# Optimization experiments

Hardware: AMD Instinct MI355X
Metric: run time of the kernel (lower is better)

The kernel has to match this reference:

```python
import jax, jax.numpy as jnp
import numpy as np

NEG_SLOPE = 0.01  # torch.nn.LeakyReLU default


def setup_inputs() -> dict:
    key = jax.random.key(0)
    ks = jax.random.split(key, 9)
    B, S, F1, F2, N, M, E, L = 2, 256, 512, 512, 20000, 2, 320000, 3
    x = jax.random.normal(ks[0], (B, S, F1), dtype=jnp.float32)
    nodes = jax.random.normal(ks[1], (N, M, F2), dtype=jnp.float32)
    edge_index = jax.random.randint(ks[2], (2, E), 0, N, dtype=jnp.int32)
    Wp = jax.random.normal(ks[3], (F1, F2), dtype=jnp.float32) * 0.02  # torch Linear weight [out,in]
    bp = jax.random.normal(ks[4], (F1,), dtype=jnp.float32) * 0.02
    gcn_W = jax.random.normal(ks[5], (L, S, S), dtype=jnp.float32) * 0.05  # stored as [in,out]
    gcn_b = jax.random.normal(ks[6], (L, S), dtype=jnp.float32) * 0.02
    w_bp = jax.random.normal(ks[7], (S,), dtype=jnp.float32) * 0.05
    b_bp = jax.random.normal(ks[8], (1,), dtype=jnp.float32) * 0.02
    return {"x": x, "nodes": nodes, "edge_index": edge_index, "Wp": Wp, "bp": bp,
            "gcn_W": gcn_W, "gcn_b": gcn_b, "w_bp": w_bp, "b_bp": b_bp}


def reference(x, nodes, edge_index, Wp, bp, gcn_W, gcn_b, w_bp, b_bp):
    # Eval mode: dropout layers are identity.
    N = nodes.shape[0]
    L = gcn_W.shape[0]
    proj = nodes @ Wp.T + bp                         # [N, M, F1]
    score = jnp.einsum('bsk,nmk->bsn', x, proj)      # sum over M and F1 -> [B, S, N]
    h = score.transpose(0, 2, 1)                     # beliefs [B, N, S]

    # GCN normalization with self-loops: D^{-1/2} (A + I) D^{-1/2}
    src, dst = edge_index[0], edge_index[1]
    loop = jnp.arange(N, dtype=edge_index.dtype)
    row = jnp.concatenate([src, loop])               # message sources
    col = jnp.concatenate([dst, loop])               # message targets
    deg = jnp.zeros((N,), dtype=h.dtype).at[col].add(1.0)
    dinv = deg ** -0.5                               # deg >= 1 due to self-loops
    norm = dinv[row] * dinv[col]                     # [E+N]

    for l in range(L):
        hw = h @ gcn_W[l]                            # [B, N, S]
        msg = hw[:, row, :] * norm[None, :, None]    # gather + scale
        agg = jnp.zeros_like(hw).at[:, col, :].add(msg) + gcn_b[l]
        h = jax.nn.leaky_relu(agg, NEG_SLOPE)

    # belief_projection: Linear(S, 1) then squeeze -> [B, N]
    return h @ w_bp + b_bp[0]
```

## Files before the change

### kernel.cpp

```cpp
#include <hip/hip_runtime.h>
#include <cstddef>
#include <cstdint>

#define NN 20000
#define SDIM 256

typedef short frag16 __attribute__((ext_vector_type(8)));
typedef float f32x4 __attribute__((ext_vector_type(4)));

__device__ inline unsigned short f32_to_bf16(float f) {
    uint32_t u = __float_as_uint(f);
    u += 0x7FFFu + ((u >> 16) & 1u);
    return (unsigned short)(u >> 16);
}

__device__ inline float4 dec4(uint2 v) {
    float4 r;
    r.x = __uint_as_float(v.x << 16);
    r.y = __uint_as_float(v.x & 0xffff0000u);
    r.z = __uint_as_float(v.y << 16);
    r.w = __uint_as_float(v.y & 0xffff0000u);
    return r;
}

__global__ __launch_bounds__(256) void prep(
    const float* __restrict__ nodes, const float* __restrict__ x,
    const float* __restrict__ Wp, const float* __restrict__ gcn_W,
    const int* __restrict__ src, const int* __restrict__ dst,
    unsigned short* __restrict__ nsum16, unsigned short* __restrict__ Wpb,
    unsigned short* __restrict__ WT, unsigned short* __restrict__ Tb,
    int* __restrict__ cnt, int* __restrict__ csr, int E)
{
    __shared__ __align__(16) char shmem[8704];
    const int blk = blockIdx.x, tid = threadIdx.x;

    if (blk < 64) {
        float* As = (float*)shmem;
        float* Bs = As + 1024;
        int b = blk >> 5, rem = blk & 31;
        int s0 = (rem >> 3) * 64, f0 = (rem & 7) * 64;
        const float* W1 = gcn_W;
        const float* xb = x + (size_t)b * 256 * 512;
        int kk = tid >> 4, c4 = (tid & 15) << 2;
        int tm = tid >> 4, tn = tid & 15;
        float acc[4][4] = {};
        for (int k0 = 0; k0 < 256; k0 += 16) {
            float4 av = *(const float4*)(W1 + (size_t)(k0 + kk) * 256 + s0 + c4);
            float4 bv = *(const float4*)(xb + (size_t)(k0 + kk) * 512 + f0 + c4);
            __syncthreads();
            *(float4*)&As[kk * 64 + c4] = av;
            *(float4*)&Bs[kk * 64 + c4] = bv;
            __syncthreads();
            #pragma unroll
            for (int k = 0; k < 16; ++k) {
                float a[4], bb[4];
                *(float4*)a  = *(const float4*)&As[k * 64 + (tm << 2)];
                *(float4*)bb = *(const float4*)&Bs[k * 64 + (tn << 2)];
                #pragma unroll
                for (int i = 0; i < 4; ++i)
                    #pragma unroll
                    for (int j = 0; j < 4; ++j) acc[i][j] += a[i] * bb[j];
            }
        }
        #pragma unroll
        for (int i = 0; i < 4; ++i) {
            int row = b * 256 + s0 + (tm << 2) + i;
            ushort4 o;
            o.x = f32_to_bf16(acc[i][0]); o.y = f32_to_bf16(acc[i][1]);
            o.z = f32_to_bf16(acc[i][2]); o.w = f32_to_bf16(acc[i][3]);
            *(ushort4*)(Tb + (size_t)row * 512 + f0 + (tn << 2)) = o;
        }
    } else if (blk < 10112) {
        int idx = (blk - 64) * 256 + tid;
        int n = idx >> 7, k4 = (idx & 127) << 2;
        uint2 o;
        if (n < NN) {
            float4 a = *(const float4*)(nodes + (size_t)n * 1024 + k4);
            float4 b = *(const float4*)(nodes + (size_t)n * 1024 + 512 + k4);
            o.x = ((uint32_t)f32_to_bf16(a.y + b.y) << 16) | f32_to_bf16(a.x + b.x);
            o.y = ((uint32_t)f32_to_bf16(a.w + b.w) << 16) | f32_to_bf16(a.z + b.z);
        } else { o.x = 0; o.y = 0; }
        *(uint2*)(nsum16 + (size_t)idx * 4) = o;
    } else if (blk < 10240) {
        size_t off = ((size_t)(blk - 10112) * 256 + tid) * 8;
        float4 a = *(const float4*)(Wp + off);
        float4 b = *(const float4*)(Wp + off + 4);
        uint4 o;
        o.x = ((uint32_t)f32_to_bf16(a.y) << 16) | f32_to_bf16(a.x);
        o.y = ((uint32_t)f32_to_bf16(a.w) << 16) | f32_to_bf16(a.z);
        o.z = ((uint32_t)f32_to_bf16(b.y) << 16) | f32_to_bf16(b.x);
        o.w = ((uint32_t)f32_to_bf16(b.w) << 16) | f32_to_bf16(b.z);
        *(uint4*)(Wpb + off) = o;
    } else if (blk < 10272) {
        unsigned short (*tsh)[68] = (unsigned short(*)[68])shmem;
        int t = blk - 10240;
        int l = t >> 4, rem = t & 15;
        int c0 = (rem & 3) * 64, r0 = (rem >> 2) * 64;
        const float* inp = gcn_W + (size_t)(l + 1) * 65536;
        unsigned short* outp = WT + (size_t)l * 65536;
        int tx = tid & 15, ty = tid >> 4;
        #pragma unroll
        for (int rr = 0; rr < 4; ++rr) {
            int r = ty * 4 + rr;
            float4 v = *(const float4*)(inp + (size_t)(r0 + r) * 256 + c0 + tx * 4);
            tsh[tx * 4 + 0][r] = f32_to_bf16(v.x);
            tsh[tx * 4 + 1][r] = f32_to_bf16(v.y);
            tsh[tx * 4 + 2][r] = f32_to_bf16(v.z);
            tsh[tx * 4 + 3][r] = f32_to_bf16(v.w);
        }
        __syncthreads();
        #pragma unroll
        for (int cc = 0; cc < 4; ++cc) {
            int c = ty * 4 + cc;
            ushort4 o = *(ushort4*)&tsh[c][tx * 4];
            *(ushort4*)(outp + (size_t)(c0 + c) * 256 + r0 + tx * 4) = o;
        }
    } else {
        int e = (blk - 10272) * 256 + tid;
        if (e < E) {
            int d = dst[e];
            int pos = atomicAdd(&cnt[d], 1);
            if (pos < 64) csr[(d << 6) + pos] = src[e];
        }
    }
}

__global__ __launch_bounds__(256) void mgemm(
    const unsigned short* __restrict__ A, const unsigned short* __restrict__ BT,
    int K, int N, int mode,
    const float* __restrict__ cb2, const int* __restrict__ cnt,
    unsigned short* __restrict__ C,
    float* __restrict__ cb2out, const float* __restrict__ bp,
    const unsigned short* __restrict__ Tb)
{
    if (mode == 0 && (int)blockIdx.y == 157) {
        int idx = blockIdx.x * 256 + threadIdx.x;
        if (idx < 512) {
            const unsigned short* tr = Tb + (size_t)idx * 512;
            float s = 0.f;
            for (int k = 0; k < 512; k += 8) {
                uint4 u = *(const uint4*)(tr + k);
                float4 a = dec4(make_uint2(u.x, u.y)), b = dec4(make_uint2(u.z, u.w));
                float4 p0 = *(const float4*)(bp + k);
                float4 p1 = *(const float4*)(bp + k + 4);
                s += a.x * p0.x + a.y * p0.y + a.z * p0.z + a.w * p0.w
                   + b.x * p1.x + b.y * p1.y + b.z * p1.z + b.w * p1.w;
            }
            cb2out[idx] = 2.0f * s;
        }
        return;
    }

    __shared__ __align__(16) unsigned short As[128 * 32];
    __shared__ __align__(16) unsigned short Bs[128 * 32];
    const int bm = blockIdx.y * 128, bn = blockIdx.x * 128;
    const int tid = threadIdx.x;
    const int lane = tid & 63, w = tid >> 6;
    const int wm = (w >> 1) << 6, wn = (w & 1) << 6;
    const int r = lane & 15, q = lane >> 4;

    f32x4 acc[4][4] = {};

    for (int k0 = 0; k0 < K; k0 += 32) {
        __syncthreads();
        #pragma unroll
        for (int t = 0; t < 2; ++t) {
            int c = t * 256 + w * 64 + lane;
            int row = c >> 2, col = (c & 3) << 3;
            __builtin_amdgcn_global_load_lds(
                (const __attribute__((address_space(1))) void*)(A + (size_t)(bm + row) * K + k0 + col),
                (__attribute__((address_space(3))) void*)(As + (size_t)(t * 256 + w * 64) * 8),
                16, 0, 0);
            __builtin_amdgcn_global_load_lds(
                (const __attribute__((address_space(1))) void*)(BT + (size_t)(bn + row) * K + k0 + col),
                (__attribute__((address_space(3))) void*)(Bs + (size_t)(t * 256 + w * 64) * 8),
                16, 0, 0);
        }
        __syncthreads();
        frag16 af[4], bf[4];
        #pragma unroll
        for (int i = 0; i < 4; ++i)
            af[i] = *(const frag16*)(As + ((wm + i * 16 + r) << 5) + (q << 3));
        #pragma unroll
        for (int j = 0; j < 4; ++j)
            bf[j] = *(const frag16*)(Bs + ((wn + j * 16 + r) << 5) + (q << 3));
        #pragma unroll
        for (int i = 0; i < 4; ++i)
            #pragma unroll
            for (int j = 0; j < 4; ++j)
                acc[i][j] = __builtin_amdgcn_mfma_f32_16x16x32_bf16(af[i], bf[j], acc[i][j], 0, 0, 0);
    }

    #pragma unroll
    for (int i = 0; i < 4; ++i) {
        #pragma unroll
        for (int rg = 0; rg < 4; ++rg) {
            int m = bm + wm + i * 16 + (q << 2) + rg;
            float sc = 1.0f;
            int b2 = 0, node = m;
            if (mode == 1) {
                int nc = m > NN - 1 ? NN - 1 : m;
                sc = rsqrtf((float)cnt[nc] + 1.0f);
            } else if (mode == 2) {
                b2 = m >= NN;
                node = m - b2 * NN;
                int nc = node > NN - 1 ? NN - 1 : node;
                sc = rsqrtf((float)cnt[nc] + 1.0f);
            }
            #pragma unroll
            for (int j = 0; j < 4; ++j) {
                int n = bn + wn + j * 16 + r;
                if (mode == 1) {
                    float v = (acc[i][j][rg] + cb2[n]) * sc;
                    C[(size_t)m * 512 + n] = f32_to_bf16(v);
                } else if (mode == 2) {
                    float v = acc[i][j][rg] * sc;
                    C[(size_t)node * 512 + (b2 << 8) + n] = f32_to_bf16(v);
                } else {
                    C[(size_t)m * N + n] = f32_to_bf16(acc[i][j][rg]);
                }
            }
        }
    }
}

__global__ __launch_bounds__(256) void aggregate_i(
    const unsigned short* __restrict__ hw, const int* __restrict__ cnt,
    const int* __restrict__ csr, const float* __restrict__ bias,
    unsigned short* __restrict__ hout,
    const float* __restrict__ w_bp, const float* __restrict__ b_bp,
    float* __restrict__ out)
{
    int n = blockIdx.x * 4 + (threadIdx.x >> 6);
    int lane = threadIdx.x & 63;
    const unsigned short* rowp = hw + (lane << 3);

    float acc[8];
    {
        uint4 u = *(const uint4*)(rowp + (size_t)n * 512);
        float4 a = dec4(make_uint2(u.x, u.y)), b = dec4(make_uint2(u.z, u.w));
        acc[0] = a.x; acc[1] = a.y; acc[2] = a.z; acc[3] = a.w;
        acc[4] = b.x; acc[5] = b.y; acc[6] = b.z; acc[7] = b.w;
    }
    int deg = cnt[n]; if (deg > 64) deg = 64;
    const int* cp = csr + (n << 6);
    int e = 0;
    for (; e + 8 <= deg; e += 8) {
        uint4 u[8];
        #pragma unroll
        for (int t = 0; t < 8; ++t)
            u[t] = *(const uint4*)(rowp + (size_t)cp[e + t] * 512);
        #pragma unroll
        for (int t = 0; t < 8; ++t) {
            float4 a = dec4(make_uint2(u[t].x, u[t].y)), b = dec4(make_uint2(u[t].z, u[t].w));
            acc[0] += a.x; acc[1] += a.y; acc[2] += a.z; acc[3] += a.w;
            acc[4] += b.x; acc[5] += b.y; acc[6] += b.z; acc[7] += b.w;
        }
    }
    if (e + 4 <= deg) {
        uint4 u[4];
        #pragma unroll
        for (int t = 0; t < 4; ++t)
            u[t] = *(const uint4*)(rowp + (size_t)cp[e + t] * 512);
        #pragma unroll
        for (int t = 0; t < 4; ++t) {
            float4 a = dec4(make_uint2(u[t].x, u[t].y)), b = dec4(make_uint2(u[t].z, u[t].w));
            acc[0] += a.x; acc[1] += a.y; acc[2] += a.z; acc[3] += a.w;
            acc[4] += b.x; acc[5] += b.y; acc[6] += b.z; acc[7] += b.w;
        }
        e += 4;
    }
    for (; e < deg; ++e) {
        uint4 u = *(const uint4*)(rowp + (size_t)cp[e] * 512);
        float4 a = dec4(make_uint2(u.x, u.y)), b = dec4(make_uint2(u.z, u.w));
        acc[0] += a.x; acc[1] += a.y; acc[2] += a.z; acc[3] += a.w;
        acc[4] += b.x; acc[5] += b.y; acc[6] += b.z; acc[7] += b.w;
    }

    float dn = rsqrtf((float)deg + 1.0f);
    int s = (lane & 31) << 3;
    float4 bl0 = *(const float4*)(bias + s);
    float4 bl1 = *(const float4*)(bias + s + 4);
    float v[8];
    v[0] = fmaf(dn, acc[0], bl0.x); v[1] = fmaf(dn, acc[1], bl0.y);
    v[2] = fmaf(dn, acc[2], bl0.z); v[3] = fmaf(dn, acc[3], bl0.w);
    v[4] = fmaf(dn, acc[4], bl1.x); v[5] = fmaf(dn, acc[5], bl1.y);
    v[6] = fmaf(dn, acc[6], bl1.z); v[7] = fmaf(dn, acc[7], bl1.w);
    #pragma unroll
    for (int j = 0; j < 8; ++j) v[j] = v[j] > 0.f ? v[j] : 0.01f * v[j];

    int b = lane >> 5;
    if (out) {
        float4 w0 = *(const float4*)(w_bp + s);
        float4 w1 = *(const float4*)(w_bp + s + 4);
        float sum = v[0] * w0.x + v[1] * w0.y + v[2] * w0.z + v[3] * w0.w
                  + v[4] * w1.x + v[5] * w1.y + v[6] * w1.z + v[7] * w1.w;
        #pragma unroll
        for (int off = 16; off; off >>= 1) sum += __shfl_xor(sum, off);
        if ((lane & 31) == 0) out[b * NN + n] = sum + b_bp[0];
    } else {
        uint4 o;
        o.x = ((uint32_t)f32_to_bf16(v[1]) << 16) | f32_to_bf16(v[0]);
        o.y = ((uint32_t)f32_to_bf16(v[3]) << 16) | f32_to_bf16(v[2]);
        o.z = ((uint32_t)f32_to_bf16(v[5]) << 16) | f32_to_bf16(v[4]);
        o.w = ((uint32_t)f32_to_bf16(v[7]) << 16) | f32_to_bf16(v[6]);
        *(uint4*)(hout + ((size_t)(b * NN + n)) * 256 + s) = o;
    }
}

extern "C" void kernel_launch(void* const* d_in, const int* in_sizes, int n_in,
                              void* d_out, int out_size, void* d_ws, size_t ws_size,
                              hipStream_t stream) {
    const float* x     = (const float*)d_in[0];
    const float* nodes = (const float*)d_in[1];
    const int*   eidx  = (const int*)d_in[2];
    const float* Wp    = (const float*)d_in[3];
    const float* bp    = (const float*)d_in[4];
    const float* gcn_W = (const float*)d_in[5];
    const float* gcn_b = (const float*)d_in[6];
    const float* w_bp  = (const float*)d_in[7];
    const float* b_bp  = (const float*)d_in[8];
    const int E = in_sizes[2] / 2;

    char* w = (char*)d_ws;
    auto alloc = [&](size_t bytes) { char* p = w; w += (bytes + 255) & ~(size_t)255; return p; };
    unsigned short* nsum16 = (unsigned short*)alloc((size_t)20096 * 512 * 2);
    unsigned short* Z      = (unsigned short*)alloc((size_t)20096 * 512 * 2);
    unsigned short* hA     = (unsigned short*)alloc((size_t)40192 * 256 * 2);
    unsigned short* hB     = (unsigned short*)alloc((size_t)40192 * 256 * 2);
    unsigned short* Wpb = (unsigned short*)alloc((size_t)512 * 512 * 2);
    unsigned short* Tb  = (unsigned short*)alloc((size_t)512 * 512 * 2);
    unsigned short* WT  = (unsigned short*)alloc((size_t)2 * 256 * 256 * 2);
    float* cb2 = (float*)alloc(512 * 4);
    int*   cnt = (int*)alloc((size_t)NN * 4);
    int*   csr = (int*)alloc((size_t)NN * 64 * 4);
    unsigned short* hw16 = nsum16;

    hipMemsetAsync(cnt, 0, (size_t)NN * 4, stream);

    const int cntBlks = (E + 255) / 256;
    prep<<<10272 + cntBlks, 256, 0, stream>>>(nodes, x, Wp, gcn_W, eidx, eidx + E,
                                              nsum16, Wpb, WT, Tb, cnt, csr, E);

    mgemm<<<dim3(4, 158), 256, 0, stream>>>(nsum16, Wpb, 512, 512, 0,
                                            nullptr, cnt, Z, cb2, bp, Tb);
    mgemm<<<dim3(4, 157), 256, 0, stream>>>(Z, Tb, 512, 512, 1,
                                            cb2, cnt, hw16, nullptr, nullptr, nullptr);

    aggregate_i<<<5000, 256, 0, stream>>>(hw16, cnt, csr, gcn_b + 0, hA,
                                          w_bp, b_bp, nullptr);
    mgemm<<<dim3(2, 313), 256, 0, stream>>>(hA, WT, 256, 256, 2,
                                            nullptr, cnt, hw16, nullptr, nullptr, nullptr);
    aggregate_i<<<5000, 256, 0, stream>>>(hw16, cnt, csr, gcn_b + 256, hB,
                                          w_bp, b_bp, nullptr);
    mgemm<<<dim3(2, 313), 256, 0, stream>>>(hB, WT + 65536, 256, 256, 2,
                                            nullptr, cnt, hw16, nullptr, nullptr, nullptr);
    aggregate_i<<<5000, 256, 0, stream>>>(hw16, cnt, csr, gcn_b + 512, nullptr,
                                          w_bp, b_bp, (float*)d_out);
}
```

Measured before the change: 393.2 us.

## Reassociate projection chain to fold Wp into small matrix, drop big GEMM

```diff
diff --git a/kernel.cpp b/kernel.cpp
--- a/kernel.cpp
+++ b/kernel.cpp
@@ -3,7 +3,6 @@
 #include <cstdint>
 
 #define NN 20000
-#define SDIM 256
 
 typedef short frag16 __attribute__((ext_vector_type(8)));
 typedef float f32x4 __attribute__((ext_vector_type(4)));
@@ -25,10 +24,10 @@
 
 __global__ __launch_bounds__(256) void prep(
     const float* __restrict__ nodes, const float* __restrict__ x,
-    const float* __restrict__ Wp, const float* __restrict__ gcn_W,
+    const float* __restrict__ gcn_W, const float* __restrict__ bp,
     const int* __restrict__ src, const int* __restrict__ dst,
-    unsigned short* __restrict__ nsum16, unsigned short* __restrict__ Wpb,
-    unsigned short* __restrict__ WT, unsigned short* __restrict__ Tb,
+    unsigned short* __restrict__ nsum16, unsigned short* __restrict__ WT,
+    float* __restrict__ Tf, float* __restrict__ cvec,
     int* __restrict__ cnt, int* __restrict__ csr, int E)
 {
     __shared__ __align__(16) char shmem[8704];
@@ -65,35 +64,36 @@
         #pragma unroll
         for (int i = 0; i < 4; ++i) {
             int row = b * 256 + s0 + (tm << 2) + i;
-            ushort4 o;
-            o.x = f32_to_bf16(acc[i][0]); o.y = f32_to_bf16(acc[i][1]);
-            o.z = f32_to_bf16(acc[i][2]); o.w = f32_to_bf16(acc[i][3]);
-            *(ushort4*)(Tb + (size_t)row * 512 + f0 + (tn << 2)) = o;
-        }
-    } else if (blk < 10112) {
-        int idx = (blk - 64) * 256 + tid;
-        int n = idx >> 7, k4 = (idx & 127) << 2;
-        uint2 o;
+            *(float4*)(Tf + (size_t)row * 512 + f0 + (tn << 2)) =
+                make_float4(acc[i][0], acc[i][1], acc[i][2], acc[i][3]);
+        }
+    } else if (blk < 2576) {
+        int g = (blk - 64) * 256 + tid;
+        int n = g >> 5, c = (g & 31) << 4;
+        uint4 o0, o1;
         if (n < NN) {
-            float4 a = *(const float4*)(nodes + (size_t)n * 1024 + k4);
-            float4 b = *(const float4*)(nodes + (size_t)n * 1024 + 512 + k4);
-            o.x = ((uint32_t)f32_to_bf16(a.y + b.y) << 16) | f32_to_bf16(a.x + b.x);
-            o.y = ((uint32_t)f32_to_bf16(a.w + b.w) << 16) | f32_to_bf16(a.z + b.z);
-        } else { o.x = 0; o.y = 0; }
-        *(uint2*)(nsum16 + (size_t)idx * 4) = o;
-    } else if (blk < 10240) {
-        size_t off = ((size_t)(blk - 10112) * 256 + tid) * 8;
-        float4 a = *(const float4*)(Wp + off);
-        float4 b = *(const float4*)(Wp + off + 4);
-        uint4 o;
-        o.x = ((uint32_t)f32_to_bf16(a.y) << 16) | f32_to_bf16(a.x);
-        o.y = ((uint32_t)f32_to_bf16(a.w) << 16) | f32_to_bf16(a.z);
-        o.z = ((uint32_t)f32_to_bf16(b.y) << 16) | f32_to_bf16(b.x);
-        o.w = ((uint32_t)f32_to_bf16(b.w) << 16) | f32_to_bf16(b.z);
-        *(uint4*)(Wpb + off) = o;
-    } else if (blk < 10272) {
+            const float* r0 = nodes + (size_t)n * 1024 + c;
+            const float* r1 = r0 + 512;
+            float4 a0 = *(const float4*)(r0 + 0),  a1 = *(const float4*)(r0 + 4);
+            float4 a2 = *(const float4*)(r0 + 8),  a3 = *(const float4*)(r0 + 12);
+            float4 b0 = *(const float4*)(r1 + 0),  b1 = *(const float4*)(r1 + 4);
+            float4 b2 = *(const float4*)(r1 + 8),  b3 = *(const float4*)(r1 + 12);
+            o0.x = ((uint32_t)f32_to_bf16(a0.y + b0.y) << 16) | f32_to_bf16(a0.x + b0.x);
+            o0.y = ((uint32_t)f32_to_bf16(a0.w + b0.w) << 16) | f32_to_bf16(a0.z + b0.z);
+            o0.z = ((uint32_t)f32_to_bf16(a1.y + b1.y) << 16) | f32_to_bf16(a1.x + b1.x);
+            o0.w = ((uint32_t)f32_to_bf16(a1.w + b1.w) << 16) | f32_to_bf16(a1.z + b1.z);
+            o1.x = ((uint32_t)f32_to_bf16(a2.y + b2.y) << 16) | f32_to_bf16(a2.x + b2.x);
+            o1.y = ((uint32_t)f32_to_bf16(a2.w + b2.w) << 16) | f32_to_bf16(a2.z + b2.z);
+            o1.z = ((uint32_t)f32_to_bf16(a3.y + b3.y) << 16) | f32_to_bf16(a3.x + b3.x);
+            o1.w = ((uint32_t)f32_to_bf16(a3.w + b3.w) << 16) | f32_to_bf16(a3.z + b3.z);
+        } else {
+            o0 = make_uint4(0, 0, 0, 0); o1 = o0;
+        }
+        *(uint4*)(nsum16 + (size_t)n * 512 + c) = o0;
+        *(uint4*)(nsum16 + (size_t)n * 512 + c + 8) = o1;
+    } else if (blk < 2608) {
         unsigned short (*tsh)[68] = (unsigned short(*)[68])shmem;
-        int t = blk - 10240;
+        int t = blk - 2576;
         int l = t >> 4, rem = t & 15;
         int c0 = (rem & 3) * 64, r0 = (rem >> 2) * 64;
         const float* inp = gcn_W + (size_t)(l + 1) * 65536;
@@ -115,8 +115,18 @@
             ushort4 o = *(ushort4*)&tsh[c][tx * 4];
             *(ushort4*)(outp + (size_t)(c0 + c) * 256 + r0 + tx * 4) = o;
         }
+    } else if (blk < 2736) {
+        int row = (blk - 2608) * 4 + (tid >> 6);
+        int lane = tid & 63;
+        const float* xr = x + (size_t)row * 512;
+        float s = 0.f;
+        #pragma unroll
+        for (int k = 0; k < 512; k += 64) s += xr[k + lane] * bp[k + lane];
+        #pragma unroll
+        for (int off = 32; off; off >>= 1) s += __shfl_down(s, off);
+        if (lane == 0) cvec[row] = 2.0f * s;
     } else {
-        int e = (blk - 10272) * 256 + tid;
+        int e = (blk - 2736) * 256 + tid;
         if (e < E) {
             int d = dst[e];
             int pos = atomicAdd(&cnt[d], 1);
@@ -125,32 +135,63 @@
     }
 }
 
+__global__ __launch_bounds__(256) void mid(
+    const float* __restrict__ Tf, const float* __restrict__ Wp,
+    const float* __restrict__ gcn_W, const float* __restrict__ cvec,
+    unsigned short* __restrict__ Ub, float* __restrict__ cb2)
+{
+    const int blk = blockIdx.x, tid = threadIdx.x;
+    if (blk >= 64) {
+        int idx = (blk - 64) * 256 + tid;
+        int b = idx >> 8, s = idx & 255;
+        float sum = 0.f;
+        for (int sp = 0; sp < 256; ++sp)
+            sum += gcn_W[(size_t)sp * 256 + s] * cvec[b * 256 + sp];
+        cb2[idx] = sum;
+        return;
+    }
+    __shared__ float As[16][68];
+    __shared__ float Bs[16][64];
+    int bm = (blk >> 3) * 64, bn = (blk & 7) * 64;
+    int arow = tid >> 2, acol = (tid & 3) << 2;
+    int brow = tid >> 4, bcol = (tid & 15) << 2;
+    int tm = tid >> 4, tn = tid & 15;
+    float acc[4][4] = {};
+    for (int k0 = 0; k0 < 512; k0 += 16) {
+        float4 av = *(const float4*)(Tf + (size_t)(bm + arow) * 512 + k0 + acol);
+        float4 bv = *(const float4*)(Wp + (size_t)(k0 + brow) * 512 + bn + bcol);
+        __syncthreads();
+        As[acol + 0][arow] = av.x; As[acol + 1][arow] = av.y;
+        As[acol + 2][arow] = av.z; As[acol + 3][arow] = av.w;
+        *(float4*)&Bs[brow][bcol] = bv;
+        __syncthreads();
+        #pragma unroll
+        for (int k = 0; k < 16; ++k) {
+            float a[4], b[4];
+            *(float4*)a = *(const float4*)&As[k][tm << 2];
+            *(float4*)b = *(const float4*)&Bs[k][tn << 2];
+            #pragma unroll
+            for (int i = 0; i < 4; ++i)
+                #pragma unroll
+                for (int j = 0; j < 4; ++j) acc[i][j] += a[i] * b[j];
+        }
+    }
+    #pragma unroll
+    for (int i = 0; i < 4; ++i) {
+        int row = bm + (tm << 2) + i;
+        ushort4 o;
+        o.x = f32_to_bf16(acc[i][0]); o.y = f32_to_bf16(acc[i][1]);
+        o.z = f32_to_bf16(acc[i][2]); o.w = f32_to_bf16(acc[i][3]);
+        *(ushort4*)(Ub + (size_t)row * 512 + bn + (tn << 2)) = o;
+    }
+}
+
 __global__ __launch_bounds__(256) void mgemm(
     const unsigned short* __restrict__ A, const unsigned short* __restrict__ BT,
     int K, int N, int mode,
     const float* __restrict__ cb2, const int* __restrict__ cnt,
-    unsigned short* __restrict__ C,
-    float* __restrict__ cb2out, const float* __restrict__ bp,
-    const unsigned short* __restrict__ Tb)
+    unsigned short* __restrict__ C)
 {
-    if (mode == 0 && (int)blockIdx.y == 157) {
-        int idx = blockIdx.x * 256 + threadIdx.x;
-        if (idx < 512) {
-            const unsigned short* tr = Tb + (size_t)idx * 512;
-            float s = 0.f;
-            for (int k = 0; k < 512; k += 8) {
-                uint4 u = *(const uint4*)(tr + k);
-                float4 a = dec4(make_uint2(u.x, u.y)), b = dec4(make_uint2(u.z, u.w));
-                float4 p0 = *(const float4*)(bp + k);
-                float4 p1 = *(const float4*)(bp + k + 4);
-                s += a.x * p0.x + a.y * p0.y + a.z * p0.z + a.w * p0.w
-                   + b.x * p1.x + b.y * p1.y + b.z * p1.z + b.w * p1.w;
-            }
-            cb2out[idx] = 2.0f * s;
-        }
-        return;
-    }
-
     __shared__ __align__(16) unsigned short As[128 * 32];
     __shared__ __align__(16) unsigned short Bs[128 * 32];
     const int bm = blockIdx.y * 128, bn = blockIdx.x * 128;
@@ -196,16 +237,17 @@
         #pragma unroll
         for (int rg = 0; rg < 4; ++rg) {
             int m = bm + wm + i * 16 + (q << 2) + rg;
-            float sc = 1.0f;
+            float sc;
             int b2 = 0, node = m;
             if (mode == 1) {
                 int nc = m > NN - 1 ? NN - 1 : m;
                 sc = rsqrtf((float)cnt[nc] + 1.0f);
-            } else if (mode == 2) {
+            } else {
                 b2 = m >= NN;
                 node = m - b2 * NN;
                 int nc = node > NN - 1 ? NN - 1 : node;
                 sc = rsqrtf((float)cnt[nc] + 1.0f);
+                if (node > 20095) node = 20095;
             }
             #pragma unroll
             for (int j = 0; j < 4; ++j) {
@@ -213,18 +255,16 @@
                 if (mode == 1) {
                     float v = (acc[i][j][rg] + cb2[n]) * sc;
                     C[(size_t)m * 512 + n] = f32_to_bf16(v);
-                } else if (mode == 2) {
+                } else {
                     float v = acc[i][j][rg] * sc;
                     C[(size_t)node * 512 + (b2 << 8) + n] = f32_to_bf16(v);
-                } else {
-                    C[(size_t)m * N + n] = f32_to_bf16(acc[i][j][rg]);
                 }
             }
         }
     }
 }
 
-__global__ __launch_bounds__(256) void aggregate_i(
+__global__ __launch_bounds__(256) void aggregate_s(
     const unsigned short* __restrict__ hw, const int* __restrict__ cnt,
     const int* __restrict__ csr, const float* __restrict__ bias,
     unsigned short* __restrict__ hout,
@@ -232,79 +272,59 @@
     float* __restrict__ out)
 {
     int n = blockIdx.x * 4 + (threadIdx.x >> 6);
+    int b = blockIdx.y;
     int lane = threadIdx.x & 63;
-    const unsigned short* rowp = hw + (lane << 3);
-
-    float acc[8];
-    {
-        uint4 u = *(const uint4*)(rowp + (size_t)n * 512);
-        float4 a = dec4(make_uint2(u.x, u.y)), b = dec4(make_uint2(u.z, u.w));
-        acc[0] = a.x; acc[1] = a.y; acc[2] = a.z; acc[3] = a.w;
-        acc[4] = b.x; acc[5] = b.y; acc[6] = b.z; acc[7] = b.w;
-    }
+    const unsigned short* rowp = hw + (b << 8) + (lane << 2);
+
+    float4 acc = dec4(*(const uint2*)(rowp + (size_t)n * 512));
     int deg = cnt[n]; if (deg > 64) deg = 64;
     const int* cp = csr + (n << 6);
     int e = 0;
     for (; e + 8 <= deg; e += 8) {
-        uint4 u[8];
-        #pragma unroll
-        for (int t = 0; t < 8; ++t)
-            u[t] = *(const uint4*)(rowp + (size_t)cp[e + t] * 512);
-        #pragma unroll
-        for (int t = 0; t < 8; ++t) {
-            float4 a = dec4(make_uint2(u[t].x, u[t].y)), b = dec4(make_uint2(u[t].z, u[t].w));
-            acc[0] += a.x; acc[1] += a.y; acc[2] += a.z; acc[3] += a.w;
-            acc[4] += b.x; acc[5] += b.y; acc[6] += b.z; acc[7] += b.w;
-        }
-    }
-    if (e + 4 <= deg) {
-        uint4 u[4];
-        #pragma unroll
-        for (int t = 0; t < 4; ++t)
-            u[t] = *(const uint4*)(rowp + (size_t)cp[e + t] * 512);
-        #pragma unroll
-        for (int t = 0; t < 4; ++t) {
-            float4 a = dec4(make_uint2(u[t].x, u[t].y)), b = dec4(make_uint2(u[t].z, u[t].w));
-            acc[0] += a.x; acc[1] += a.y; acc[2] += a.z; acc[3] += a.w;
-            acc[4] += b.x; acc[5] += b.y; acc[6] += b.z; acc[7] += b.w;
-        }
-        e += 4;
+        int4 c0 = *(const int4*)(cp + e);
+        int4 c1 = *(const int4*)(cp + e + 4);
+        uint2 u0 = *(const uint2*)(rowp + (size_t)c0.x * 512);
+        uint2 u1 = *(const uint2*)(rowp + (size_t)c0.y * 512);
+        uint2 u2 = *(const uint2*)(rowp + (size_t)c0.z * 512);
+        uint2 u3 = *(const uint2*)(rowp + (size_t)c0.w * 512);
+        uint2 u4 = *(const uint2*)(rowp + (size_t)c1.x * 512);
+        uint2 u5 = *(const uint2*)(rowp + (size_t)c1.y * 512);
+        uint2 u6 = *(const uint2*)(rowp + (size_t)c1.z * 512);
+        uint2 u7 = *(const uint2*)(rowp + (size_t)c1.w * 512);
+        float4 f0 = dec4(u0), f1 = dec4(u1), f2 = dec4(u2), f3 = dec4(u3);
+        float4 f4 = dec4(u4), f5 = dec4(u5), f6 = dec4(u6), f7 = dec4(u7);
+        acc.x += ((f0.x + f1.x) + (f2.x + f3.x)) + ((f4.x + f5.x) + (f6.x + f7.x));
+        acc.y += ((f0.y + f1.y) + (f2.y + f3.y)) + ((f4.y + f5.y) + (f6.y + f7.y));
+        acc.z += ((f0.z + f1.z) + (f2.z + f3.z)) + ((f4.z + f5.z) + (f6.z + f7.z));
+        acc.w += ((f0.w + f1.w) + (f2.w + f3.w)) + ((f4.w + f5.w) + (f6.w + f7.w));
     }
     for (; e < deg; ++e) {
-        uint4 u = *(const uint4*)(rowp + (size_t)cp[e] * 512);
-        float4 a = dec4(make_uint2(u.x, u.y)), b = dec4(make_uint2(u.z, u.w));
-        acc[0] += a.x; acc[1] += a.y; acc[2] += a.z; acc[3] += a.w;
-        acc[4] += b.x; acc[5] += b.y; acc[6] += b.z; acc[7] += b.w;
+        float4 f = dec4(*(const uint2*)(rowp + (size_t)cp[e] * 512));
+        acc.x += f.x; acc.y += f.y; acc.z += f.z; acc.w += f.w;
     }
 
     float dn = rsqrtf((float)deg + 1.0f);
-    int s = (lane & 31) << 3;
-    float4 bl0 = *(const float4*)(bias + s);
-    float4 bl1 = *(const float4*)(bias + s + 4);
-    float v[8];
-    v[0] = fmaf(dn, acc[0], bl0.x); v[1] = fmaf(dn, acc[1], bl0.y);
-    v[2] = fmaf(dn, acc[2], bl0.z); v[3] = fmaf(dn, acc[3], bl0.w);
-    v[4] = fmaf(dn, acc[4], bl1.x); v[5] = fmaf(dn, acc[5], bl1.y);
-    v[6] = fmaf(dn, acc[6], bl1.z); v[7] = fmaf(dn, acc[7], bl1.w);
-    #pragma unroll
-    for (int j = 0; j < 8; ++j) v[j] = v[j] > 0.f ? v[j] : 0.01f * v[j];
-
-    int b = lane >> 5;
+    int s = lane << 2;
+    float4 bl = *(const float4*)(bias + s);
+    float4 v;
+    v.x = fmaf(dn, acc.x, bl.x); v.y = fmaf(dn, acc.y, bl.y);
+    v.z = fmaf(dn, acc.z, bl.z); v.w = fmaf(dn, acc.w, bl.w);
+    v.x = v.x > 0.f ? v.x : 0.01f * v.x;
+    v.y = v.y > 0.f ? v.y : 0.01f * v.y;
+    v.z = v.z > 0.f ? v.z : 0.01f * v.z;
+    v.w = v.w > 0.f ? v.w : 0.01f * v.w;
+
     if (out) {
-        float4 w0 = *(const float4*)(w_bp + s);
-        float4 w1 = *(const float4*)(w_bp + s + 4);
-        float sum = v[0] * w0.x + v[1] * w0.y + v[2] * w0.z + v[3] * w0.w
-                  + v[4] * w1.x + v[5] * w1.y + v[6] * w1.z + v[7] * w1.w;
-        #pragma unroll
-        for (int off = 16; off; off >>= 1) sum += __shfl_xor(sum, off);
-        if ((lane & 31) == 0) out[b * NN + n] = sum + b_bp[0];
+        float4 w4 = *(const float4*)(w_bp + s);
+        float sum = v.x * w4.x + v.y * w4.y + v.z * w4.z + v.w * w4.w;
+        #pragma unroll
+        for (int off = 32; off; off >>= 1) sum += __shfl_xor(sum, off);
+        if (lane == 0) out[b * NN + n] = sum + b_bp[0];
     } else {
-        uint4 o;
-        o.x = ((uint32_t)f32_to_bf16(v[1]) << 16) | f32_to_bf16(v[0]);
-        o.y = ((uint32_t)f32_to_bf16(v[3]) << 16) | f32_to_bf16(v[2]);
-        o.z = ((uint32_t)f32_to_bf16(v[5]) << 16) | f32_to_bf16(v[4]);
-        o.w = ((uint32_t)f32_to_bf16(v[7]) << 16) | f32_to_bf16(v[6]);
-        *(uint4*)(hout + ((size_t)(b * NN + n)) * 256 + s) = o;
+        uint2 o;
+        o.x = ((uint32_t)f32_to_bf16(v.y) << 16) | f32_to_bf16(v.x);
+        o.y = ((uint32_t)f32_to_bf16(v.w) << 16) | f32_to_bf16(v.z);
+        *(uint2*)(hout + ((size_t)(b * NN + n)) * 256 + s) = o;
     }
 }
 
@@ -325,36 +345,32 @@
     char* w = (char*)d_ws;
     auto alloc = [&](size_t bytes) { char* p = w; w += (bytes + 255) & ~(size_t)255; return p; };
     unsigned short* nsum16 = (unsigned short*)alloc((size_t)20096 * 512 * 2);
-    unsigned short* Z      = (unsigned short*)alloc((size_t)20096 * 512 * 2);
+    unsigned short* hw16   = (unsigned short*)alloc((size_t)20096 * 512 * 2);
     unsigned short* hA     = (unsigned short*)alloc((size_t)40192 * 256 * 2);
     unsigned short* hB     = (unsigned short*)alloc((size_t)40192 * 256 * 2);
-    unsigned short* Wpb = (unsigned short*)alloc((size_t)512 * 512 * 2);
-    unsigned short* Tb  = (unsigned short*)alloc((size_t)512 * 512 * 2);
-    unsigned short* WT  = (unsigned short*)alloc((size_t)2 * 256 * 256 * 2);
-    float* cb2 = (float*)alloc(512 * 4);
-    int*   cnt = (int*)alloc((size_t)NN * 4);
-    int*   csr = (int*)alloc((size_t)NN * 64 * 4);
-    unsigned short* hw16 = nsum16;
+    float* Tf  = (float*)alloc((size_t)512 * 512 * 4);
+    unsigned short* Ub = (unsigned short*)alloc((size_t)512 * 512 * 2);
+    unsigned short* WT = (unsigned short*)alloc((size_t)2 * 256 * 256 * 2);
+    float* cvec = (float*)alloc(512 * 4);
+    float* cb2  = (float*)alloc(512 * 4);
+    int*   cnt  = (int*)alloc((size_t)NN * 4);
+    int*   csr  = (int*)alloc((size_t)NN * 64 * 4);
 
     hipMemsetAsync(cnt, 0, (size_t)NN * 4, stream);
 
     const int cntBlks = (E + 255) / 256;
-    prep<<<10272 + cntBlks, 256, 0, stream>>>(nodes, x, Wp, gcn_W, eidx, eidx + E,
-                                              nsum16, Wpb, WT, Tb, cnt, csr, E);
-
-    mgemm<<<dim3(4, 158), 256, 0, stream>>>(nsum16, Wpb, 512, 512, 0,
-                                            nullptr, cnt, Z, cb2, bp, Tb);
-    mgemm<<<dim3(4, 157), 256, 0, stream>>>(Z, Tb, 512, 512, 1,
-                                            cb2, cnt, hw16, nullptr, nullptr, nullptr);
-
-    aggregate_i<<<5000, 256, 0, stream>>>(hw16, cnt, csr, gcn_b + 0, hA,
-                                          w_bp, b_bp, nullptr);
-    mgemm<<<dim3(2, 313), 256, 0, stream>>>(hA, WT, 256, 256, 2,
-                                            nullptr, cnt, hw16, nullptr, nullptr, nullptr);
-    aggregate_i<<<5000, 256, 0, stream>>>(hw16, cnt, csr, gcn_b + 256, hB,
-                                          w_bp, b_bp, nullptr);
-    mgemm<<<dim3(2, 313), 256, 0, stream>>>(hB, WT + 65536, 256, 256, 2,
-                                            nullptr, cnt, hw16, nullptr, nullptr, nullptr);
-    aggregate_i<<<5000, 256, 0, stream>>>(hw16, cnt, csr, gcn_b + 512, nullptr,
-                                          w_bp, b_bp, (float*)d_out);
-}
+    prep<<<2736 + cntBlks, 256, 0, stream>>>(nodes, x, gcn_W, bp, eidx, eidx + E,
+                                             nsum16, WT, Tf, cvec, cnt, csr, E);
+    mid<<<66, 256, 0, stream>>>(Tf, Wp, gcn_W, cvec, Ub, cb2);
+
+    mgemm<<<dim3(4, 157), 256, 0, stream>>>(nsum16, Ub, 512, 512, 1, cb2, cnt, hw16);
+
+    aggregate_s<<<dim3(5000, 2), 256, 0, stream>>>(hw16, cnt, csr, gcn_b + 0, hA,
+                                                   w_bp, b_bp, nullptr);
+    mgemm<<<dim3(2, 313), 256, 0, stream>>>(hA, WT, 256, 256, 2, nullptr, cnt, hw16);
+    aggregate_s<<<dim3(5000, 2), 256, 0, stream>>>(hw16, cnt, csr, gcn_b + 256, hB,
+                                                   w_bp, b_bp, nullptr);
+    mgemm<<<dim3(2, 313), 256, 0, stream>>>(hB, WT + 65536, 256, 256, 2, nullptr, cnt, hw16);
+    aggregate_s<<<dim3(5000, 2), 256, 0, stream>>>(hw16, cnt, csr, gcn_b + 512, nullptr,
+                                                   w_bp, b_bp, (float*)d_out);
+}
```

Measured after the change: 388.5 us. About the same (-1.2%).
